# Kernel optimization log

Measured on AMD Instinct MI355X. Metric: run time of the kernel, lower is better.

Reference implementation:

```python
import jax, jax.numpy as jnp
import numpy as np

B, HQ, HKV, D = 32, 32, 8, 128
BLOCK_SIZE, MAX_BLOCKS = 16, 128
NUM_BLOCKS = B * MAX_BLOCKS
LMAX = MAX_BLOCKS * BLOCK_SIZE  # 2048 max context per sequence
ROPE_BASE = 10000.0


def _rope(x, pos):
    """Apply rotary embedding. x: [B, H, D], pos: [B] int positions."""
    half = D // 2
    inv_freq = 1.0 / (ROPE_BASE ** (jnp.arange(0, D, 2, dtype=jnp.float32) / D))  # [D/2]
    freqs = pos.astype(jnp.float32)[:, None] * inv_freq[None, :]  # [B, D/2]
    emb = jnp.concatenate([freqs, freqs], axis=-1)                # [B, D]
    cos = jnp.cos(emb)[:, None, :]  # [B, 1, D]
    sin = jnp.sin(emb)[:, None, :]
    x1, x2 = x[..., :half], x[..., half:]
    rotated = jnp.concatenate([-x2, x1], axis=-1)
    return x * cos + rotated * sin


def setup_inputs() -> dict:
    key = jax.random.key(0)
    ks = jax.random.split(key, 6)
    query = jax.random.normal(ks[0], (B, HQ, D), jnp.float32)
    new_k = jax.random.normal(ks[1], (B, HKV, D), jnp.float32)
    new_v = jax.random.normal(ks[2], (B, HKV, D), jnp.float32)
    k_cache = jax.random.normal(ks[3], (NUM_BLOCKS, BLOCK_SIZE, HKV, D), jnp.float32)
    v_cache = jax.random.normal(ks[4], (NUM_BLOCKS, BLOCK_SIZE, HKV, D), jnp.float32)
    # each sequence owns a disjoint contiguous range of blocks
    block_table = jnp.arange(B * MAX_BLOCKS, dtype=jnp.int32).reshape(B, MAX_BLOCKS)
    context_lens = jax.random.randint(ks[5], (B,), 1, LMAX - 1).astype(jnp.int32)
    return dict(query=query, new_k=new_k, new_v=new_v, k_cache=k_cache,
                v_cache=v_cache, block_table=block_table, context_lens=context_lens)


def reference(query, new_k, new_v, k_cache, v_cache, block_table, context_lens):
    scale = 1.0 / D ** 0.5
    pos = context_lens  # new token position for each sequence, [B]

    # RoPE on the decode-step query and key (seq_len == 1 per sequence)
    q = _rope(query, pos)      # [B, HQ, D]
    k_new = _rope(new_k, pos)  # [B, HKV, D]

    # flatten paged cache to [NUM_BLOCKS*BLOCK_SIZE, HKV, D]
    kc = k_cache.reshape(-1, HKV, D)
    vc = v_cache.reshape(-1, HKV, D)

    # paged KV-cache append: slot = block_table[b, pos//bs]*bs + pos%bs
    blk_new = jnp.take_along_axis(block_table, (pos // BLOCK_SIZE)[:, None], axis=1)[:, 0]
    slot = blk_new * BLOCK_SIZE + pos % BLOCK_SIZE  # [B]
    kc = kc.at[slot].set(k_new)
    vc = vc.at[slot].set(new_v)

    # gather per-sequence K/V via block table: [B, LMAX, HKV, D]
    p = jnp.arange(LMAX, dtype=jnp.int32)
    blks = block_table[:, p // BLOCK_SIZE]                 # [B, LMAX]
    idx = blks * BLOCK_SIZE + (p % BLOCK_SIZE)[None, :]    # [B, LMAX]
    keys = kc[idx]
    vals = vc[idx]

    # GQA attention over valid context (lengths = context_lens + 1 after append)
    lens = pos + 1
    g = HQ // HKV
    qg = q.reshape(B, HKV, g, D)
    scores = jnp.einsum('bkgd,blkd->bkgl', qg, keys) * scale  # [B, HKV, g, LMAX]
    mask = p[None, :] < lens[:, None]  # [B, LMAX]
    scores = jnp.where(mask[:, None, None, :], scores, -jnp.inf)
    w = jax.nn.softmax(scores, axis=-1)
    out = jnp.einsum('bkgl,blkd->bkgd', w, vals)
    return out.reshape(B, HQ, D)
```

## Files before the change

kernel.cpp:

```cpp
#include <hip/hip_runtime.h>
#include <math.h>

#define BATCH 32
#define HQ 32
#define HKV 8
#define DHEAD 128
#define BS 16
#define MAXB 128
#define G 4
#define CHUNK 128
#define MAXCH 16
#define NW 4
#define NT (NW * 64)

#define NSLOT (BATCH * HKV * MAXCH)
#define NBKV  (BATCH * HKV)

typedef float v2f __attribute__((ext_vector_type(2)));

__device__ __forceinline__ v2f pk_fma(v2f a, v2f b, v2f c) {
    v2f d;
    asm("v_pk_fma_f32 %0, %1, %2, %3" : "=v"(d) : "v"(a), "v"(b), "v"(c));
    return d;
}
__device__ __forceinline__ v2f pk_mul(v2f a, v2f b) {
    v2f d;
    asm("v_pk_mul_f32 %0, %1, %2" : "=v"(d) : "v"(a), "v"(b));
    return d;
}
__device__ __forceinline__ float fexp2(float x) {
    float r;
    asm("v_exp_f32 %0, %1" : "=v"(r) : "v"(x));
    return r;
}

#define ROR4(N, x0, x1, x2, x3)                                                   \
    asm("s_nop 1\n\t"                                                             \
        "v_add_f32_dpp %0, %0, %0 row_ror:" #N " row_mask:0xf bank_mask:0xf\n\t"  \
        "v_add_f32_dpp %1, %1, %1 row_ror:" #N " row_mask:0xf bank_mask:0xf\n\t"  \
        "v_add_f32_dpp %2, %2, %2 row_ror:" #N " row_mask:0xf bank_mask:0xf\n\t"  \
        "v_add_f32_dpp %3, %3, %3 row_ror:" #N " row_mask:0xf bank_mask:0xf"      \
        : "+v"(x0), "+v"(x1), "+v"(x2), "+v"(x3))

__global__ __launch_bounds__(128) void paged_attn_prep(
    const float* __restrict__ query,
    const float* __restrict__ new_k,
    const float* __restrict__ new_v,
    const int*   __restrict__ context_lens,
    float* __restrict__ qs,
    float* __restrict__ kn,
    float* __restrict__ vn)
{
    const int bkv = blockIdx.x;
    const int kv  = bkv & 7;
    const int b   = bkv >> 3;
    const int tid = threadIdx.x;

    __shared__ float s_cos[64], s_sin[64];
    const int pos = context_lens[b];
    if (tid < 64) {
        float invf = exp2f((float)tid * -0.20762050593046014f);
        float ang  = (float)pos * invf;
        s_cos[tid] = cosf(ang);
        s_sin[tid] = sinf(ang);
    }
    __syncthreads();

    const float scale = 0.08838834764831845f * 1.4426950408889634f;

    for (int idx = tid; idx < G * DHEAD; idx += 128) {
        int h = idx >> 7, d = idx & 127;
        const float* qp = query + ((size_t)b * HQ + kv * G + h) * DHEAD;
        float x = qp[d], r;
        if (d < 64) r = x * s_cos[d]      - qp[d + 64] * s_sin[d];
        else        r = x * s_cos[d - 64] + qp[d - 64] * s_sin[d - 64];
        qs[(size_t)bkv * (G * DHEAD) + idx] = r * scale;
    }
    {
        int d = tid;
        const float* kp = new_k + ((size_t)b * HKV + kv) * DHEAD;
        float x = kp[d], r;
        if (d < 64) r = x * s_cos[d]      - kp[d + 64] * s_sin[d];
        else        r = x * s_cos[d - 64] + kp[d - 64] * s_sin[d - 64];
        kn[(size_t)bkv * DHEAD + d] = r;
        vn[(size_t)bkv * DHEAD + d] = new_v[((size_t)b * HKV + kv) * DHEAD + d];
    }
}

__global__ __launch_bounds__(NT) void paged_attn_chunk(
    const float* __restrict__ k_cache,
    const float* __restrict__ v_cache,
    const int*   __restrict__ block_table,
    const int*   __restrict__ context_lens,
    const float* __restrict__ qs,
    const float* __restrict__ kn,
    const float* __restrict__ vn,
    float*       __restrict__ wsacc,
    float*       __restrict__ wsl)
{
    const int c   = blockIdx.x & (MAXCH - 1);
    const int bkv = blockIdx.x >> 4;
    const int kv  = bkv & 7;
    const int b   = bkv >> 3;

    const int pos = context_lens[b];
    const int c0  = c << 7;
    if (c0 > pos) return;

    const int tid  = threadIdx.x;
    const int w    = tid >> 6;
    const int lane = tid & 63;
    const int grp  = lane >> 4;
    const int sub  = lane & 15;

    __shared__ float s_wacc[NW][G][DHEAD];
    __shared__ float s_wl[NW][G];

    v2f q2[G][4];
    const float* qb = qs + (size_t)bkv * (G * DHEAD) + sub * 8;
    #pragma unroll
    for (int h = 0; h < G; h++) {
        float4 qa = *(const float4*)(qb + h * DHEAD);
        float4 qc = *(const float4*)(qb + h * DHEAD + 4);
        q2[h][0] = v2f{qa.x, qa.y}; q2[h][1] = v2f{qa.z, qa.w};
        q2[h][2] = v2f{qc.x, qc.y}; q2[h][3] = v2f{qc.z, qc.w};
    }

    const int tb  = b * MAXB + (c0 >> 4) + w * 2;
    const int bt0 = __builtin_amdgcn_readfirstlane(block_table[tb]);
    const int bt1 = __builtin_amdgcn_readfirstlane(block_table[tb + 1]);

    const int poff = grp * (HKV * DHEAD) + kv * DHEAD + sub * 8;
    const float* kb0 = k_cache + (size_t)bt0 * (BS * HKV * DHEAD) + poff;
    const float* kb1 = k_cache + (size_t)bt1 * (BS * HKV * DHEAD) + poff;
    const float* vb0 = v_cache + (size_t)bt0 * (BS * HKV * DHEAD) + poff;
    const float* vb1 = v_cache + (size_t)bt1 * (BS * HKV * DHEAD) + poff;

    const float* knp = kn + (size_t)bkv * DHEAD + sub * 8;
    const float* vnp = vn + (size_t)bkv * DHEAD + sub * 8;

    const int p0 = c0 + w * 32 + grp;

    v2f acc2[G][4];
    float l[G];
    #pragma unroll
    for (int h = 0; h < G; h++) {
        l[h] = 0.f;
        #pragma unroll
        for (int j = 0; j < 4; j++) acc2[h][j] = v2f{0.f, 0.f};
    }

    float4 kaA, kbA, vaA, vbA;
    float4 kaB, kbB, vaB, vbB;

#define LOADSET(KA, KB, VA, VB, IT) do {                                       \
        const float* kp_ = ((IT) < 4 ? kb0 : kb1) + ((IT) & 3) * 4096;         \
        const float* vp_ = ((IT) < 4 ? vb0 : vb1) + ((IT) & 3) * 4096;         \
        KA = *(const float4*)kp_;  KB = *(const float4*)(kp_ + 4);             \
        VA = *(const float4*)vp_;  VB = *(const float4*)(vp_ + 4);             \
    } while (0)

#define COMPSET(KA, KB, VA, VB, IT) do {                                       \
        const int pi_ = p0 + (IT) * 4;                                         \
        if (__builtin_expect(pi_ == pos, 0)) {      \
            KA = *(const float4*)(knp);  KB = *(const float4*)(knp + 4);       \
            VA = *(const float4*)(vnp);  VB = *(const float4*)(vnp + 4);       \
        }                                                                      \
        v2f k0_ = v2f{KA.x, KA.y}, k1_ = v2f{KA.z, KA.w};                      \
        v2f k2_ = v2f{KB.x, KB.y}, k3_ = v2f{KB.z, KB.w};                      \
        v2f d0_ = pk_fma(q2[0][3], k3_, pk_fma(q2[0][2], k2_,                  \
                  pk_fma(q2[0][1], k1_, pk_mul(q2[0][0], k0_))));              \
        v2f d1_ = pk_fma(q2[1][3], k3_, pk_fma(q2[1][2], k2_,                  \
                  pk_fma(q2[1][1], k1_, pk_mul(q2[1][0], k0_))));              \
        v2f d2_ = pk_fma(q2[2][3], k3_, pk_fma(q2[2][2], k2_,                  \
                  pk_fma(q2[2][1], k1_, pk_mul(q2[2][0], k0_))));              \
        v2f d3_ = pk_fma(q2[3][3], k3_, pk_fma(q2[3][2], k2_,                  \
                  pk_fma(q2[3][1], k1_, pk_mul(q2[3][0], k0_))));              \
        float dt0 = d0_.x + d0_.y, dt1 = d1_.x + d1_.y;                        \
        float dt2 = d2_.x + d2_.y, dt3 = d3_.x + d3_.y;                        \
        ROR4(8, dt0, dt1, dt2, dt3);                                           \
        ROR4(4, dt0, dt1, dt2, dt3);                                           \
        ROR4(2, dt0, dt1, dt2, dt3);                                           \
        ROR4(1, dt0, dt1, dt2, dt3);                                           \
        const bool act_ = pi_ <= pos;                                          \
        float wg0 = act_ ? fexp2(dt0) : 0.f;                                   \
        float wg1 = act_ ? fexp2(dt1) : 0.f;                                   \
        float wg2 = act_ ? fexp2(dt2) : 0.f;                                   \
        float wg3 = act_ ? fexp2(dt3) : 0.f;                                   \
        l[0] += wg0; l[1] += wg1; l[2] += wg2; l[3] += wg3;                    \
        v2f u0_ = v2f{VA.x, VA.y}, u1_ = v2f{VA.z, VA.w};                      \
        v2f u2_ = v2f{VB.x, VB.y}, u3_ = v2f{VB.z, VB.w};                      \
        v2f w0_ = v2f{wg0, wg0}, w1_ = v2f{wg1, wg1};                          \
        v2f w2_ = v2f{wg2, wg2}, w3_ = v2f{wg3, wg3};                          \
        acc2[0][0] = pk_fma(w0_, u0_, acc2[0][0]);                             \
        acc2[0][1] = pk_fma(w0_, u1_, acc2[0][1]);                             \
        acc2[0][2] = pk_fma(w0_, u2_, acc2[0][2]);                             \
        acc2[0][3] = pk_fma(w0_, u3_, acc2[0][3]);                             \
        acc2[1][0] = pk_fma(w1_, u0_, acc2[1][0]);                             \
        acc2[1][1] = pk_fma(w1_, u1_, acc2[1][1]);                             \
        acc2[1][2] = pk_fma(w1_, u2_, acc2[1][2]);                             \
        acc2[1][3] = pk_fma(w1_, u3_, acc2[1][3]);                             \
        acc2[2][0] = pk_fma(w2_, u0_, acc2[2][0]);                             \
        acc2[2][1] = pk_fma(w2_, u1_, acc2[2][1]);                             \
        acc2[2][2] = pk_fma(w2_, u2_, acc2[2][2]);                             \
        acc2[2][3] = pk_fma(w2_, u3_, acc2[2][3]);                             \
        acc2[3][0] = pk_fma(w3_, u0_, acc2[3][0]);                             \
        acc2[3][1] = pk_fma(w3_, u1_, acc2[3][1]);                             \
        acc2[3][2] = pk_fma(w3_, u2_, acc2[3][2]);                             \
        acc2[3][3] = pk_fma(w3_, u3_, acc2[3][3]);                             \
    } while (0)

    LOADSET(kaA, kbA, vaA, vbA, 0);
    LOADSET(kaB, kbB, vaB, vbB, 1);
    COMPSET(kaA, kbA, vaA, vbA, 0);  LOADSET(kaA, kbA, vaA, vbA, 2);
    COMPSET(kaB, kbB, vaB, vbB, 1);  LOADSET(kaB, kbB, vaB, vbB, 3);
    COMPSET(kaA, kbA, vaA, vbA, 2);  LOADSET(kaA, kbA, vaA, vbA, 4);
    COMPSET(kaB, kbB, vaB, vbB, 3);  LOADSET(kaB, kbB, vaB, vbB, 5);
    COMPSET(kaA, kbA, vaA, vbA, 4);  LOADSET(kaA, kbA, vaA, vbA, 6);
    COMPSET(kaB, kbB, vaB, vbB, 5);  LOADSET(kaB, kbB, vaB, vbB, 7);
    COMPSET(kaA, kbA, vaA, vbA, 6);
    COMPSET(kaB, kbB, vaB, vbB, 7);

#undef LOADSET
#undef COMPSET

    #pragma unroll
    for (int h = 0; h < G; h++) {
        l[h] += __shfl_xor(l[h], 16, 64);
        l[h] += __shfl_xor(l[h], 32, 64);
        #pragma unroll
        for (int j = 0; j < 4; j++) {
            float ax = acc2[h][j].x, ay = acc2[h][j].y;
            ax += __shfl_xor(ax, 16, 64); ax += __shfl_xor(ax, 32, 64);
            ay += __shfl_xor(ay, 16, 64); ay += __shfl_xor(ay, 32, 64);
            acc2[h][j] = v2f{ax, ay};
        }
    }
    if (lane < 16) {
        #pragma unroll
        for (int h = 0; h < G; h++)
            #pragma unroll
            for (int j = 0; j < 4; j++) {
                s_wacc[w][h][sub * 8 + 2 * j]     = acc2[h][j].x;
                s_wacc[w][h][sub * 8 + 2 * j + 1] = acc2[h][j].y;
            }
    }
    if (lane == 0) {
        #pragma unroll
        for (int h = 0; h < G; h++) s_wl[w][h] = l[h];
    }
    __syncthreads();

    const size_t slot_base = (size_t)blockIdx.x * (G * DHEAD);
    for (int idx = tid; idx < G * DHEAD; idx += NT) {
        float s = s_wacc[0][idx >> 7][idx & 127] + s_wacc[1][idx >> 7][idx & 127]
                + s_wacc[2][idx >> 7][idx & 127] + s_wacc[3][idx >> 7][idx & 127];
        wsacc[slot_base + idx] = s;
    }
    if (tid < G) {
        wsl[(size_t)blockIdx.x * G + tid] =
            s_wl[0][tid] + s_wl[1][tid] + s_wl[2][tid] + s_wl[3][tid];
    }
}

__global__ __launch_bounds__(512) void paged_attn_combine(
    const int*   __restrict__ context_lens,
    const float* __restrict__ wsacc,
    const float* __restrict__ wsl,
    float*       __restrict__ out)
{
    const int bkv = blockIdx.x;
    const int kv  = bkv & 7;
    const int b   = bkv >> 3;
    const int t   = threadIdx.x;
    const int h   = t >> 7;
    const int d   = t & 127;

    const int len = context_lens[b] + 1;
    const int nch = (len + CHUNK - 1) >> 7;

    float asum = 0.f, lsum = 0.f;
    for (int cc = 0; cc < nch; cc++) {
        asum += wsacc[((size_t)bkv * MAXCH + cc) * (G * DHEAD) + t];
        lsum += wsl[((size_t)bkv * MAXCH + cc) * G + h];
    }
    out[((size_t)b * HQ + kv * G + h) * DHEAD + d] = asum / lsum;
}

extern "C" void kernel_launch(void* const* d_in, const int* in_sizes, int n_in,
                              void* d_out, int out_size, void* d_ws, size_t ws_size,
                              hipStream_t stream) {
    const float* query        = (const float*)d_in[0];
    const float* new_k        = (const float*)d_in[1];
    const float* new_v        = (const float*)d_in[2];
    const float* k_cache      = (const float*)d_in[3];
    const float* v_cache      = (const float*)d_in[4];
    const int*   block_table  = (const int*)d_in[5];
    const int*   context_lens = (const int*)d_in[6];
    float* out = (float*)d_out;

    float* wsacc = (float*)d_ws;
    float* wsl   = wsacc + (size_t)NSLOT * G * DHEAD;
    float* qs    = wsl + (size_t)NSLOT * G;
    float* kn    = qs + (size_t)NBKV * G * DHEAD;
    float* vn    = kn + (size_t)NBKV * DHEAD;

    paged_attn_prep<<<dim3(NBKV), dim3(128), 0, stream>>>(
        query, new_k, new_v, context_lens, qs, kn, vn);
    paged_attn_chunk<<<dim3(NSLOT), dim3(NT), 0, stream>>>(
        k_cache, v_cache, block_table, context_lens, qs, kn, vn, wsacc, wsl);
    paged_attn_combine<<<dim3(NBKV), dim3(512), 0, stream>>>(
        context_lens, wsacc, wsl, out);
}
```

Baseline: 85.29 us.

## Double chunk size and move new-token key/value handling into combine kernel

```diff
diff --git a/kernel.cpp b/kernel.cpp
--- a/kernel.cpp
+++ b/kernel.cpp
@@ -8,8 +8,8 @@
 #define BS 16
 #define MAXB 128
 #define G 4
-#define CHUNK 128
-#define MAXCH 16
+#define CHUNK 256
+#define MAXCH 8
 #define NW 4
 #define NT (NW * 64)
 
@@ -44,12 +44,8 @@
 
 __global__ __launch_bounds__(128) void paged_attn_prep(
     const float* __restrict__ query,
-    const float* __restrict__ new_k,
-    const float* __restrict__ new_v,
     const int*   __restrict__ context_lens,
-    float* __restrict__ qs,
-    float* __restrict__ kn,
-    float* __restrict__ vn)
+    float* __restrict__ qs)
 {
     const int bkv = blockIdx.x;
     const int kv  = bkv & 7;
@@ -76,15 +72,6 @@
         else        r = x * s_cos[d - 64] + qp[d - 64] * s_sin[d - 64];
         qs[(size_t)bkv * (G * DHEAD) + idx] = r * scale;
     }
-    {
-        int d = tid;
-        const float* kp = new_k + ((size_t)b * HKV + kv) * DHEAD;
-        float x = kp[d], r;
-        if (d < 64) r = x * s_cos[d]      - kp[d + 64] * s_sin[d];
-        else        r = x * s_cos[d - 64] + kp[d - 64] * s_sin[d - 64];
-        kn[(size_t)bkv * DHEAD + d] = r;
-        vn[(size_t)bkv * DHEAD + d] = new_v[((size_t)b * HKV + kv) * DHEAD + d];
-    }
 }
 
 __global__ __launch_bounds__(NT) void paged_attn_chunk(
@@ -93,18 +80,16 @@
     const int*   __restrict__ block_table,
     const int*   __restrict__ context_lens,
     const float* __restrict__ qs,
-    const float* __restrict__ kn,
-    const float* __restrict__ vn,
     float*       __restrict__ wsacc,
     float*       __restrict__ wsl)
 {
     const int c   = blockIdx.x & (MAXCH - 1);
-    const int bkv = blockIdx.x >> 4;
+    const int bkv = blockIdx.x >> 3;
     const int kv  = bkv & 7;
     const int b   = bkv >> 3;
 
     const int pos = context_lens[b];
-    const int c0  = c << 7;
+    const int c0  = c << 8;
     if (c0 > pos) return;
 
     const int tid  = threadIdx.x;
@@ -126,20 +111,25 @@
         q2[h][2] = v2f{qc.x, qc.y}; q2[h][3] = v2f{qc.z, qc.w};
     }
 
-    const int tb  = b * MAXB + (c0 >> 4) + w * 2;
-    const int bt0 = __builtin_amdgcn_readfirstlane(block_table[tb]);
+    const int tb  = b * MAXB + (c0 >> 4) + w * 4;
+    const int bt0 = __builtin_amdgcn_readfirstlane(block_table[tb + 0]);
     const int bt1 = __builtin_amdgcn_readfirstlane(block_table[tb + 1]);
-
-    const int poff = grp * (HKV * DHEAD) + kv * DHEAD + sub * 8;
-    const float* kb0 = k_cache + (size_t)bt0 * (BS * HKV * DHEAD) + poff;
-    const float* kb1 = k_cache + (size_t)bt1 * (BS * HKV * DHEAD) + poff;
-    const float* vb0 = v_cache + (size_t)bt0 * (BS * HKV * DHEAD) + poff;
-    const float* vb1 = v_cache + (size_t)bt1 * (BS * HKV * DHEAD) + poff;
-
-    const float* knp = kn + (size_t)bkv * DHEAD + sub * 8;
-    const float* vnp = vn + (size_t)bkv * DHEAD + sub * 8;
-
-    const int p0 = c0 + w * 32 + grp;
+    const int bt2 = __builtin_amdgcn_readfirstlane(block_table[tb + 2]);
+    const int bt3 = __builtin_amdgcn_readfirstlane(block_table[tb + 3]);
+
+    const size_t BLKF = (size_t)BS * HKV * DHEAD;
+    const int loff = grp * (HKV * DHEAD) + kv * DHEAD + sub * 8;
+
+    const float* kparr[4] = { k_cache + bt0 * BLKF + loff,
+                              k_cache + bt1 * BLKF + loff,
+                              k_cache + bt2 * BLKF + loff,
+                              k_cache + bt3 * BLKF + loff };
+    const float* vparr[4] = { v_cache + bt0 * BLKF + loff,
+                              v_cache + bt1 * BLKF + loff,
+                              v_cache + bt2 * BLKF + loff,
+                              v_cache + bt3 * BLKF + loff };
+
+    const int p0 = c0 + w * 64 + grp;
 
     v2f acc2[G][4];
     float l[G];
@@ -154,18 +144,14 @@
     float4 kaB, kbB, vaB, vbB;
 
 #define LOADSET(KA, KB, VA, VB, IT) do {                                       \
-        const float* kp_ = ((IT) < 4 ? kb0 : kb1) + ((IT) & 3) * 4096;         \
-        const float* vp_ = ((IT) < 4 ? vb0 : vb1) + ((IT) & 3) * 4096;         \
+        const float* kp_ = kparr[(IT) >> 2] + ((IT) & 3) * (4 * HKV * DHEAD);  \
+        const float* vp_ = vparr[(IT) >> 2] + ((IT) & 3) * (4 * HKV * DHEAD);  \
         KA = *(const float4*)kp_;  KB = *(const float4*)(kp_ + 4);             \
         VA = *(const float4*)vp_;  VB = *(const float4*)(vp_ + 4);             \
     } while (0)
 
 #define COMPSET(KA, KB, VA, VB, IT) do {                                       \
         const int pi_ = p0 + (IT) * 4;                                         \
-        if (__builtin_expect(pi_ == pos, 0)) {      \
-            KA = *(const float4*)(knp);  KB = *(const float4*)(knp + 4);       \
-            VA = *(const float4*)(vnp);  VB = *(const float4*)(vnp + 4);       \
-        }                                                                      \
         v2f k0_ = v2f{KA.x, KA.y}, k1_ = v2f{KA.z, KA.w};                      \
         v2f k2_ = v2f{KB.x, KB.y}, k3_ = v2f{KB.z, KB.w};                      \
         v2f d0_ = pk_fma(q2[0][3], k3_, pk_fma(q2[0][2], k2_,                  \
@@ -182,7 +168,7 @@
         ROR4(4, dt0, dt1, dt2, dt3);                                           \
         ROR4(2, dt0, dt1, dt2, dt3);                                           \
         ROR4(1, dt0, dt1, dt2, dt3);                                           \
-        const bool act_ = pi_ <= pos;                                          \
+        const bool act_ = pi_ < pos;        \
         float wg0 = act_ ? fexp2(dt0) : 0.f;                                   \
         float wg1 = act_ ? fexp2(dt1) : 0.f;                                   \
         float wg2 = act_ ? fexp2(dt2) : 0.f;                                   \
@@ -212,14 +198,22 @@
 
     LOADSET(kaA, kbA, vaA, vbA, 0);
     LOADSET(kaB, kbB, vaB, vbB, 1);
-    COMPSET(kaA, kbA, vaA, vbA, 0);  LOADSET(kaA, kbA, vaA, vbA, 2);
-    COMPSET(kaB, kbB, vaB, vbB, 1);  LOADSET(kaB, kbB, vaB, vbB, 3);
-    COMPSET(kaA, kbA, vaA, vbA, 2);  LOADSET(kaA, kbA, vaA, vbA, 4);
-    COMPSET(kaB, kbB, vaB, vbB, 3);  LOADSET(kaB, kbB, vaB, vbB, 5);
-    COMPSET(kaA, kbA, vaA, vbA, 4);  LOADSET(kaA, kbA, vaA, vbA, 6);
-    COMPSET(kaB, kbB, vaB, vbB, 5);  LOADSET(kaB, kbB, vaB, vbB, 7);
-    COMPSET(kaA, kbA, vaA, vbA, 6);
-    COMPSET(kaB, kbB, vaB, vbB, 7);
+    COMPSET(kaA, kbA, vaA, vbA, 0);   LOADSET(kaA, kbA, vaA, vbA, 2);
+    COMPSET(kaB, kbB, vaB, vbB, 1);   LOADSET(kaB, kbB, vaB, vbB, 3);
+    COMPSET(kaA, kbA, vaA, vbA, 2);   LOADSET(kaA, kbA, vaA, vbA, 4);
+    COMPSET(kaB, kbB, vaB, vbB, 3);   LOADSET(kaB, kbB, vaB, vbB, 5);
+    COMPSET(kaA, kbA, vaA, vbA, 4);   LOADSET(kaA, kbA, vaA, vbA, 6);
+    COMPSET(kaB, kbB, vaB, vbB, 5);   LOADSET(kaB, kbB, vaB, vbB, 7);
+    COMPSET(kaA, kbA, vaA, vbA, 6);   LOADSET(kaA, kbA, vaA, vbA, 8);
+    COMPSET(kaB, kbB, vaB, vbB, 7);   LOADSET(kaB, kbB, vaB, vbB, 9);
+    COMPSET(kaA, kbA, vaA, vbA, 8);   LOADSET(kaA, kbA, vaA, vbA, 10);
+    COMPSET(kaB, kbB, vaB, vbB, 9);   LOADSET(kaB, kbB, vaB, vbB, 11);
+    COMPSET(kaA, kbA, vaA, vbA, 10);  LOADSET(kaA, kbA, vaA, vbA, 12);
+    COMPSET(kaB, kbB, vaB, vbB, 11);  LOADSET(kaB, kbB, vaB, vbB, 13);
+    COMPSET(kaA, kbA, vaA, vbA, 12);  LOADSET(kaA, kbA, vaA, vbA, 14);
+    COMPSET(kaB, kbB, vaB, vbB, 13);  LOADSET(kaB, kbB, vaB, vbB, 15);
+    COMPSET(kaA, kbA, vaA, vbA, 14);
+    COMPSET(kaB, kbB, vaB, vbB, 15);
 
 #undef LOADSET
 #undef COMPSET
@@ -264,7 +258,10 @@
 }
 
 __global__ __launch_bounds__(512) void paged_attn_combine(
+    const float* __restrict__ new_k,
+    const float* __restrict__ new_v,
     const int*   __restrict__ context_lens,
+    const float* __restrict__ qs,
     const float* __restrict__ wsacc,
     const float* __restrict__ wsl,
     float*       __restrict__ out)
@@ -275,16 +272,46 @@
     const int t   = threadIdx.x;
     const int h   = t >> 7;
     const int d   = t & 127;
-
-    const int len = context_lens[b] + 1;
-    const int nch = (len + CHUNK - 1) >> 7;
+    const int wv  = t >> 6;
+
+    __shared__ float s_cos[64], s_sin[64], s_kn[DHEAD], s_ps[8];
+
+    const int pos = context_lens[b];
+    if (t < 64) {
+        float invf = exp2f((float)t * -0.20762050593046014f);
+        float ang  = (float)pos * invf;
+        s_cos[t] = cosf(ang);
+        s_sin[t] = sinf(ang);
+    }
+    __syncthreads();
+    if (t < DHEAD) {
+        const float* kp = new_k + ((size_t)b * HKV + kv) * DHEAD;
+        float x = kp[t], r;
+        if (t < 64) r = x * s_cos[t]      - kp[t + 64] * s_sin[t];
+        else        r = x * s_cos[t - 64] + kp[t - 64] * s_sin[t - 64];
+        s_kn[t] = r;
+    }
+    __syncthreads();
+
+    float part = qs[(size_t)bkv * (G * DHEAD) + t] * s_kn[d];
+    #pragma unroll
+    for (int off = 1; off < 64; off <<= 1) part += __shfl_xor(part, off, 64);
+    if ((t & 63) == 0) s_ps[wv] = part;
+    __syncthreads();
+
+    const float wnew = fexp2(s_ps[2 * h] + s_ps[2 * h + 1]);
+
+    const int len = pos + 1;
+    const int nch = (len + CHUNK - 1) >> 8;
 
     float asum = 0.f, lsum = 0.f;
     for (int cc = 0; cc < nch; cc++) {
         asum += wsacc[((size_t)bkv * MAXCH + cc) * (G * DHEAD) + t];
         lsum += wsl[((size_t)bkv * MAXCH + cc) * G + h];
     }
-    out[((size_t)b * HQ + kv * G + h) * DHEAD + d] = asum / lsum;
+    const float vnew = new_v[((size_t)b * HKV + kv) * DHEAD + d];
+    out[((size_t)b * HQ + kv * G + h) * DHEAD + d] =
+        (asum + wnew * vnew) / (lsum + wnew);
 }
 
 extern "C" void kernel_launch(void* const* d_in, const int* in_sizes, int n_in,
@@ -302,13 +329,11 @@
     float* wsacc = (float*)d_ws;
     float* wsl   = wsacc + (size_t)NSLOT * G * DHEAD;
     float* qs    = wsl + (size_t)NSLOT * G;
-    float* kn    = qs + (size_t)NBKV * G * DHEAD;
-    float* vn    = kn + (size_t)NBKV * DHEAD;
 
     paged_attn_prep<<<dim3(NBKV), dim3(128), 0, stream>>>(
-        query, new_k, new_v, context_lens, qs, kn, vn);
+        query, context_lens, qs);
     paged_attn_chunk<<<dim3(NSLOT), dim3(NT), 0, stream>>>(
-        k_cache, v_cache, block_table, context_lens, qs, kn, vn, wsacc, wsl);
+        k_cache, v_cache, block_table, context_lens, qs, wsacc, wsl);
     paged_attn_combine<<<dim3(NBKV), dim3(512), 0, stream>>>(
-        context_lens, wsacc, wsl, out);
-}
+        new_k, new_v, context_lens, qs, wsacc, wsl, out);
+}
```

Measured after the change: 79.72 us. -6.5%, faster.
